# Performance work log

Hardware: AMD Instinct MI355X
Metric: run time of the kernel (lower is better)

The kernel has to match this reference:

```python
import jax, jax.numpy as jnp
import numpy as np

N, E = 50000, 800000
F, H, M = 64, 128, 64  # feature_dim, hidden_dim, message_dim (message_dim must equal feature_dim)


def _mlp(x, W1, b1, W2, b2):
    return jnp.maximum(x @ W1 + b1, 0.0) @ W2 + b2


def setup_inputs() -> dict:
    key = jax.random.key(0)
    ks = jax.random.split(key, 20)
    p = lambda k, s: (jax.random.normal(k, s, jnp.float32) * 0.05)
    return {
        "z_h": jax.random.normal(ks[0], (N, F), jnp.float32),
        "pos_world": jax.random.normal(ks[1], (3,), jnp.float32),
        "edge_index": jax.random.randint(ks[2], (2, E), 0, N),
        "We1": p(ks[3], (2 * F + 8, H)), "be1": p(ks[4], (H,)),
        "We2": p(ks[5], (H, M)), "be2": p(ks[6], (M,)),
        "Wg1": p(ks[7], (2 * F + 8, H)), "bg1": p(ks[8], (H,)),
        "Wg2": p(ks[9], (H, 1)), "bg2": p(ks[10], (1,)),
        "Wn1": p(ks[11], (F + M, H)), "bn1": p(ks[12], (H,)),
        "Wn2": p(ks[13], (H, F)), "bn2": p(ks[14], (F,)),
        "Ww1": p(ks[15], (F + 3, H)), "bw1": p(ks[16], (H,)),
        "Ww2": p(ks[17], (H, M)), "bw2": p(ks[18], (M,)),
    }


def reference(z_h, pos_world, edge_index,
              We1, be1, We2, be2,
              Wg1, bg1, Wg2, bg2,
              Wn1, bn1, Wn2, bn2,
              Ww1, bw1, Ww2, bw2):
    src, tgt = edge_index[0], edge_index[1]
    zs = z_h[src]  # [E, F]
    zt = z_h[tgt]  # [E, F]

    # edge features: diff(3) + dist(1) + vel cross product(3) + its norm(1)
    diff = zs[:, 0:3] - zt[:, 0:3]
    dist = jnp.sum(diff * diff, axis=-1, keepdims=True)
    cross = jnp.cross(zs[:, 3:6], zt[:, 3:6])
    cross_n = jnp.linalg.norm(cross, axis=-1, keepdims=True)
    e_feat = jnp.concatenate([diff, dist, cross, cross_n], axis=-1)  # [E, 8]

    inp_edge = jnp.concatenate([zs, zt, e_feat], axis=-1)  # [E, 2F+8]
    m = _mlp(inp_edge, We1, be1, We2, be2)                 # [E, M]
    w = jax.nn.sigmoid(_mlp(inp_edge, Wg1, bg1, Wg2, bg2))  # [E, 1]

    # scatter_add weighted messages to target nodes
    m_agg_h = jax.ops.segment_sum(w * m, tgt, num_segments=N)  # [N, F] (M == F)

    # world message: sum over all nodes, broadcast back
    diff_world = z_h[:, 0:3] - pos_world
    inp_world = jnp.concatenate([z_h, diff_world], axis=-1)  # [N, F+3]
    m_h_w = _mlp(inp_world, Ww1, bw1, Ww2, bw2)              # [N, M]
    m_agg_w = jnp.sum(m_h_w, axis=0, keepdims=True)          # [1, M] -> broadcast

    m_agg_total = m_agg_h + m_agg_w
    inp_node = jnp.concatenate([z_h, m_agg_total], axis=-1)  # [N, F+M]
    delta_z_h = _mlp(inp_node, Wn1, bn1, Wn2, bn2)           # [N, F]
    return delta_z_h
```

## Files before the change

### kernel.cpp

```cpp
#include <hip/hip_runtime.h>
#include <math.h>

#define NN 50000
#define NE 800000
#define EBLOCKS (NE / 64)
#define WBLOCKS ((NN + 63) / 64)

typedef float     f32x4  __attribute__((ext_vector_type(4)));
typedef __bf16    bf16x8 __attribute__((ext_vector_type(8)));
typedef _Float16  f16x2  __attribute__((ext_vector_type(2)));
typedef _Float16  f16x8  __attribute__((ext_vector_type(8)));

#define WE1F_OFF 0
#define WE2F_OFF 5120
#define WN1F_OFF 6144
#define WN2F_OFF 8192
#define WW1F_OFF 9216
#define WW2F_OFF 10752
#define NCHUNKS  11776


__device__ inline bf16x8 pack8(float4 a, float4 b) {
    bf16x8 r;
    r[0] = (__bf16)a.x; r[1] = (__bf16)a.y; r[2] = (__bf16)a.z; r[3] = (__bf16)a.w;
    r[4] = (__bf16)b.x; r[5] = (__bf16)b.y; r[6] = (__bf16)b.z; r[7] = (__bf16)b.w;
    return r;
}

__device__ inline void pk_atomic_add_f16(void* addr, f16x2 v) {
#if __has_builtin(__builtin_amdgcn_global_atomic_fadd_v2f16)
    __builtin_amdgcn_global_atomic_fadd_v2f16((f16x2*)addr, v);
#else
    asm volatile("global_atomic_pk_add_f16 %0, %1, off"
                 :: "v"(addr), "v"(v) : "memory");
#endif
}

__global__ __launch_bounds__(256) void prep(
    const float* __restrict__ We1, const float* __restrict__ Wg1,
    const float* __restrict__ We2, const float* __restrict__ Wn1,
    const float* __restrict__ Wn2, const float* __restrict__ Ww1,
    const float* __restrict__ Ww2, bf16x8* __restrict__ wsF,
    const float* __restrict__ z, float* __restrict__ db,
    float* __restrict__ m_agg_w)
{
    const int c = blockIdx.x * 256 + threadIdx.x;

    if (c < 64) m_agg_w[c] = 0.f;

    if (c < NN * 8) {
        int node = c >> 3, q = c & 7;
        const float4* s = (const float4*)(z + (long)node * 64) + q * 2;
        float4 a = s[0], b = s[1];
        *(bf16x8*)((char*)db + (long)node * 256 + 128 + q * 16) = pack8(a, b);
        float4 zz = {0.f, 0.f, 0.f, 0.f};
        *(float4*)((char*)db + (long)node * 256 + q * 16) = zz;
    }

    if (c >= NCHUNKS) return;
    const int lane = c & 63, l16 = lane & 15, row8 = ((lane >> 4) & 3) * 8;
    bf16x8 p;
    if (c < WE2F_OFF) {
        int ct = (c >> 6) & 15, kc = c >> 10;
        int col = ct * 16 + l16;
        const float* src = (col < 128) ? (We1 + col) : (Wg1 + (col - 128));
#pragma unroll
        for (int i = 0; i < 8; i++) {
            int r = kc * 32 + row8 + i;
            p[i] = (__bf16)((r < 136) ? src[(size_t)r * 128] : 0.f);
        }
    } else if (c < WN1F_OFF) {
        int cc = c - WE2F_OFF; int ct = (cc >> 6) & 3, kc = cc >> 8;
        int col = ct * 16 + l16;
#pragma unroll
        for (int i = 0; i < 8; i++)
            p[i] = (__bf16)We2[(size_t)(kc * 32 + row8 + i) * 64 + col];
    } else if (c < WN2F_OFF) {
        int cc = c - WN1F_OFF; int ct = (cc >> 6) & 7, kc = cc >> 9;
        int col = ct * 16 + l16;
#pragma unroll
        for (int i = 0; i < 8; i++)
            p[i] = (__bf16)Wn1[(size_t)(kc * 32 + row8 + i) * 128 + col];
    } else if (c < WW1F_OFF) {
        int cc = c - WN2F_OFF; int ct = (cc >> 6) & 3, kc = cc >> 8;
        int col = ct * 16 + l16;
#pragma unroll
        for (int i = 0; i < 8; i++)
            p[i] = (__bf16)Wn2[(size_t)(kc * 32 + row8 + i) * 64 + col];
    } else if (c < WW2F_OFF) {
        int cc = c - WW1F_OFF; int ct = (cc >> 6) & 7, kc = cc >> 9;
        int col = ct * 16 + l16;
#pragma unroll
        for (int i = 0; i < 8; i++) {
            int r = kc * 32 + row8 + i;
            p[i] = (__bf16)((r < 67) ? Ww1[(size_t)r * 128 + col] : 0.f);
        }
    } else {
        int cc = c - WW2F_OFF; int ct = (cc >> 6) & 3, kc = cc >> 8;
        int col = ct * 16 + l16;
#pragma unroll
        for (int i = 0; i < 8; i++)
            p[i] = (__bf16)Ww2[(size_t)(kc * 32 + row8 + i) * 64 + col];
    }
    wsF[c] = p;
}

union FusedLds {
    bf16x8 XF[1280];
    struct {
        bf16x8   HF[1024];
        _Float16 M[64 * 68];
    } s;
};

__global__ __launch_bounds__(512, 6) void fused_kernel(
    const float* __restrict__ z_h, const int* __restrict__ ei,
    const bf16x8* __restrict__ We1F, const bf16x8* __restrict__ We2F,
    const float* __restrict__ be1, const float* __restrict__ be2,
    const float* __restrict__ bg1, const float* __restrict__ Wg2,
    const float* __restrict__ bg2,
    const float* __restrict__ pos_world,
    const bf16x8* __restrict__ Ww1F, const bf16x8* __restrict__ Ww2F,
    const float* __restrict__ bw1, const float* __restrict__ bw2,
    float* __restrict__ magg_rows,
    float* __restrict__ m_agg_w)
{
    __shared__ FusedLds U;
    __shared__ int   tgt_s[64];
    __shared__ float gred[4][64];

    const int t = threadIdx.x;
    const int lane = t & 63, w = t >> 6;
    const int quad = lane >> 4, l16 = lane & 15;

    if (blockIdx.x >= EBLOCKS) {
        const int n0 = (blockIdx.x - EBLOCKS) * 64;
        {
            int nn = t >> 3, q = t & 7;
            int mt = nn >> 4, l16e = nn & 15;
            int node = n0 + nn; if (node >= NN) node = NN - 1;
            if (q < 4) {
                const float4* zr = (const float4*)(z_h + (long)node * 64) + q * 4;
                float4 a0 = zr[0], a1 = zr[1], a2 = zr[2], a3 = zr[3];
                int kcs = q >> 1, qa = (q & 1) * 2;
                U.XF[(kcs * 4 + mt) * 64 + qa * 16 + l16e]       = pack8(a0, a1);
                U.XF[(kcs * 4 + mt) * 64 + (qa + 1) * 16 + l16e] = pack8(a2, a3);
            } else if (q == 4) {
                float4 a0 = *(const float4*)(z_h + (long)node * 64);
                bf16x8 f;
#pragma unroll
                for (int i = 0; i < 8; i++) f[i] = (__bf16)0.f;
                f[0] = (__bf16)(a0.x - pos_world[0]);
                f[1] = (__bf16)(a0.y - pos_world[1]);
                f[2] = (__bf16)(a0.z - pos_world[2]);
                U.XF[(8 + mt) * 64 + l16e] = f;
            } else {
                bf16x8 z;
#pragma unroll
                for (int i = 0; i < 8; i++) z[i] = (__bf16)0.f;
                U.XF[(8 + mt) * 64 + (q - 4) * 16 + l16e] = z;
            }
        }
        __syncthreads();

        f32x4 acc[4];
        {
            float b = bw1[w * 16 + l16];
#pragma unroll
            for (int mt = 0; mt < 4; mt++) { f32x4 v = {b, b, b, b}; acc[mt] = v; }
        }
#pragma unroll
        for (int kc = 0; kc < 3; kc++) {
            bf16x8 bfr = Ww1F[(kc * 8 + w) * 64 + lane];
#pragma unroll
            for (int mt = 0; mt < 4; mt++)
                acc[mt] = __builtin_amdgcn_mfma_f32_16x16x32_bf16(
                    U.XF[(kc * 4 + mt) * 64 + lane], bfr, acc[mt], 0, 0, 0);
        }
        __syncthreads();

        {
            __bf16* HFp = (__bf16*)U.s.HF;
            int cw = w * 16 + l16;
            int kc2 = cw >> 5, quad2 = (cw >> 3) & 3, ii = cw & 7;
#pragma unroll
            for (int mt = 0; mt < 4; mt++)
#pragma unroll
                for (int r = 0; r < 4; r++)
                    HFp[(((kc2 * 4 + mt) * 64) + quad2 * 16 + quad * 4 + r) * 8 + ii] =
                        (__bf16)fmaxf(acc[mt][r], 0.f);
        }
        __syncthreads();

        {
            const int nt = w & 3, mh = w >> 2;
            f32x4 acc2[2];
            float b2 = bw2[nt * 16 + l16];
#pragma unroll
            for (int m = 0; m < 2; m++) { f32x4 v = {b2, b2, b2, b2}; acc2[m] = v; }
#pragma unroll
            for (int kc = 0; kc < 4; kc++) {
                bf16x8 b2f = Ww2F[(kc * 4 + nt) * 64 + lane];
#pragma unroll
                for (int m = 0; m < 2; m++)
                    acc2[m] = __builtin_amdgcn_mfma_f32_16x16x32_bf16(
                        U.s.HF[(kc * 4 + mh * 2 + m) * 64 + lane], b2f, acc2[m], 0, 0, 0);
            }
            float s = 0.f;
#pragma unroll
            for (int m = 0; m < 2; m++)
#pragma unroll
                for (int r = 0; r < 4; r++) {
                    int node = n0 + (mh * 2 + m) * 16 + quad * 4 + r;
                    s += (node < NN) ? acc2[m][r] : 0.f;
                }
            s += __shfl_xor(s, 16, 64);
            s += __shfl_xor(s, 32, 64);
            if (quad == 0) atomicAdd(m_agg_w + nt * 16 + l16, s);
        }
        return;
    }

    const int e0 = blockIdx.x * 64;

    {
        const int ee = t >> 3, q = t & 7;
        const int mt = ee >> 4, l16e = ee & 15;
        const int eg = e0 + ee;
        const int rs = ei[eg], rt = ei[NE + eg];
        const bf16x8* zs = (const bf16x8*)((const char*)magg_rows + (long)rs * 256 + 128);
        const bf16x8* zt = (const bf16x8*)((const char*)magg_rows + (long)rt * 256 + 128);
        bf16x8 sa = zs[q];
        bf16x8 ta = zt[q];
        const int kcs = q >> 2, qslot = q & 3;
        U.XF[(kcs * 4 + mt) * 64 + qslot * 16 + l16e]       = sa;
        U.XF[((kcs + 2) * 4 + mt) * 64 + qslot * 16 + l16e] = ta;
        if (q == 4) tgt_s[ee] = rt;
        if (q == 0) {
            float dx = (float)sa[0] - (float)ta[0];
            float dy = (float)sa[1] - (float)ta[1];
            float dz = (float)sa[2] - (float)ta[2];
            float ax = (float)sa[3], ay = (float)sa[4], az = (float)sa[5];
            float bx = (float)ta[3], by = (float)ta[4], bz = (float)ta[5];
            float cx = ay * bz - az * by;
            float cy = az * bx - ax * bz;
            float cz = ax * by - ay * bx;
            bf16x8 f;
            f[0] = (__bf16)dx; f[1] = (__bf16)dy; f[2] = (__bf16)dz;
            f[3] = (__bf16)(dx * dx + dy * dy + dz * dz);
            f[4] = (__bf16)cx; f[5] = (__bf16)cy; f[6] = (__bf16)cz;
            f[7] = (__bf16)sqrtf(cx * cx + cy * cy + cz * cz);
            U.XF[(16 + mt) * 64 + l16e] = f;
        } else if (q >= 5) {
            bf16x8 z;
#pragma unroll
            for (int i = 0; i < 8; i++) z[i] = (__bf16)0.f;
            U.XF[(16 + mt) * 64 + (q - 4) * 16 + l16e] = z;
        }
    }
    __syncthreads();

    f32x4 acc[4][2];
#pragma unroll
    for (int nt = 0; nt < 2; nt++) {
        int col = (w * 2 + nt) * 16 + l16;
        float b = (col < 128) ? be1[col] : bg1[col - 128];
#pragma unroll
        for (int mt = 0; mt < 4; mt++) { f32x4 v = {b, b, b, b}; acc[mt][nt] = v; }
    }
    bf16x8 bcur0 = We1F[(w * 2) * 64 + lane];
    bf16x8 bcur1 = We1F[(w * 2 + 1) * 64 + lane];
#pragma unroll
    for (int kc = 0; kc < 5; kc++) {
        bf16x8 bnx0, bnx1;
        if (kc < 4) {
            bnx0 = We1F[((kc + 1) * 16 + w * 2) * 64 + lane];
            bnx1 = We1F[((kc + 1) * 16 + w * 2 + 1) * 64 + lane];
        }
#pragma unroll
        for (int mt = 0; mt < 4; mt++) {
            bf16x8 af = U.XF[(kc * 4 + mt) * 64 + lane];
            acc[mt][0] = __builtin_amdgcn_mfma_f32_16x16x32_bf16(af, bcur0, acc[mt][0], 0, 0, 0);
            acc[mt][1] = __builtin_amdgcn_mfma_f32_16x16x32_bf16(af, bcur1, acc[mt][1], 0, 0, 0);
        }
        bcur0 = bnx0; bcur1 = bnx1;
    }
    __syncthreads();

    if (w < 4) {
        __bf16* HFp = (__bf16*)U.s.HF;
#pragma unroll
        for (int nt = 0; nt < 2; nt++) {
            int cw = (w * 2 + nt) * 16 + l16;
            int kc2 = cw >> 5, quad2 = (cw >> 3) & 3, ii = cw & 7;
#pragma unroll
            for (int mt = 0; mt < 4; mt++)
#pragma unroll
                for (int r = 0; r < 4; r++)
                    HFp[(((kc2 * 4 + mt) * 64) + quad2 * 16 + quad * 4 + r) * 8 + ii] =
                        (__bf16)fmaxf(acc[mt][nt][r], 0.f);
        }
    } else {
        float gp[4][4];
#pragma unroll
        for (int mt = 0; mt < 4; mt++)
#pragma unroll
            for (int r = 0; r < 4; r++) gp[mt][r] = 0.f;
#pragma unroll
        for (int nt = 0; nt < 2; nt++) {
            float wg = Wg2[((w - 4) * 2 + nt) * 16 + l16];
#pragma unroll
            for (int mt = 0; mt < 4; mt++)
#pragma unroll
                for (int r = 0; r < 4; r++)
                    gp[mt][r] += fmaxf(acc[mt][nt][r], 0.f) * wg;
        }
#pragma unroll
        for (int mask = 1; mask < 16; mask <<= 1)
#pragma unroll
            for (int mt = 0; mt < 4; mt++)
#pragma unroll
                for (int r = 0; r < 4; r++)
                    gp[mt][r] += __shfl_xor(gp[mt][r], mask, 64);
        if (l16 == 0) {
#pragma unroll
            for (int mt = 0; mt < 4; mt++)
#pragma unroll
                for (int r = 0; r < 4; r++)
                    gred[(w - 4) & 3][mt * 16 + quad * 4 + r] = gp[mt][r];
        }
    }
    __syncthreads();

    if (w < 4) {
        f32x4 acc2[4];
        float b2 = be2[w * 16 + l16];
#pragma unroll
        for (int mt = 0; mt < 4; mt++) { f32x4 v = {b2, b2, b2, b2}; acc2[mt] = v; }
        bf16x8 c2 = We2F[w * 64 + lane];
#pragma unroll
        for (int kc = 0; kc < 4; kc++) {
            bf16x8 n2;
            if (kc < 3) n2 = We2F[((kc + 1) * 4 + w) * 64 + lane];
#pragma unroll
            for (int mt = 0; mt < 4; mt++)
                acc2[mt] = __builtin_amdgcn_mfma_f32_16x16x32_bf16(
                    U.s.HF[(kc * 4 + mt) * 64 + lane], c2, acc2[mt], 0, 0, 0);
            c2 = n2;
        }

        float wgtreg;
        {
            float g = bg2[0] + gred[0][lane] + gred[1][lane]
                             + gred[2][lane] + gred[3][lane];
            wgtreg = 1.f / (1.f + __expf(-g));
        }

#pragma unroll
        for (int mt = 0; mt < 4; mt++)
#pragma unroll
            for (int r = 0; r < 4; r++) {
                int edge = mt * 16 + quad * 4 + r;
                float wg = __shfl(wgtreg, edge, 64);
                U.s.M[edge * 68 + w * 16 + l16] =
                    (_Float16)(acc2[mt][r] * wg);
            }
    }
    __syncthreads();

    {
        const int p = t & 31, eb = t >> 5;
        char* base = (char*)magg_rows;
#pragma unroll
        for (int k = 0; k < 4; k++) {
            int e = eb + k * 16;
            f16x2 v = *(const f16x2*)&U.s.M[e * 68 + p * 2];
            pk_atomic_add_f16(base + (long)tgt_s[e] * 256 + p * 4, v);
        }
    }
}

__global__ __launch_bounds__(512, 4) void node_kernel(
    const float* __restrict__ m_agg_w,
    const bf16x8* __restrict__ Wn1F, const bf16x8* __restrict__ Wn2F,
    const float* __restrict__ bn1, const float* __restrict__ bn2,
    float* __restrict__ outp)
{
    __shared__ bf16x8 XF[1024];
    __shared__ bf16x8 HF[1024];
    const int t = threadIdx.x;
    const int n0 = blockIdx.x * 64;
    const int lane = t & 63, w = t >> 6;
    const int quad = lane >> 4, l16 = lane & 15;

    {
        int nn = t >> 3, q = t & 7;
        int mt = nn >> 4, l16e = nn & 15;
        int node = n0 + nn; if (node >= NN) node = NN - 1;
        int half = q >> 2, sub = q & 3;
        bf16x8 c0, c1;
        if (half == 0) {
            const bf16x8* zr = (const bf16x8*)((const char*)outp + (long)node * 256 + 128) + sub * 2;
            c0 = zr[0]; c1 = zr[1];
        } else {
            const f16x8* mr = (const f16x8*)((const char*)outp + (long)node * 256) + sub * 2;
            f16x8 r0 = mr[0], r1 = mr[1];
            const float* mw = m_agg_w + sub * 16;
#pragma unroll
            for (int i = 0; i < 8; i++) {
                c0[i] = (__bf16)((float)r0[i] + mw[i]);
                c1[i] = (__bf16)((float)r1[i] + mw[i + 8]);
            }
        }
        int kcs = (sub >> 1) + half * 2, qa = (sub & 1) * 2;
        XF[(kcs * 4 + mt) * 64 + qa * 16 + l16e]       = c0;
        XF[(kcs * 4 + mt) * 64 + (qa + 1) * 16 + l16e] = c1;
    }
    __syncthreads();

    f32x4 acc[4];
    {
        float b = bn1[w * 16 + l16];
#pragma unroll
        for (int mt = 0; mt < 4; mt++) { f32x4 v = {b, b, b, b}; acc[mt] = v; }
    }
#pragma unroll
    for (int kc = 0; kc < 4; kc++) {
        bf16x8 bfr = Wn1F[(kc * 8 + w) * 64 + lane];
#pragma unroll
        for (int mt = 0; mt < 4; mt++)
            acc[mt] = __builtin_amdgcn_mfma_f32_16x16x32_bf16(
                XF[(kc * 4 + mt) * 64 + lane], bfr, acc[mt], 0, 0, 0);
    }

    {
        __bf16* HFp = (__bf16*)HF;
        int cw = w * 16 + l16;
        int kc2 = cw >> 5, quad2 = (cw >> 3) & 3, ii = cw & 7;
#pragma unroll
        for (int mt = 0; mt < 4; mt++)
#pragma unroll
            for (int r = 0; r < 4; r++)
                HFp[(((kc2 * 4 + mt) * 64) + quad2 * 16 + quad * 4 + r) * 8 + ii] =
                    (__bf16)fmaxf(acc[mt][r], 0.f);
    }
    __syncthreads();

    {
        const int nt = w & 3, mh = w >> 2;
        f32x4 acc2[2];
        float b2 = bn2[nt * 16 + l16];
#pragma unroll
        for (int m = 0; m < 2; m++) { f32x4 v = {b2, b2, b2, b2}; acc2[m] = v; }
#pragma unroll
        for (int kc = 0; kc < 4; kc++) {
            bf16x8 b2f = Wn2F[(kc * 4 + nt) * 64 + lane];
#pragma unroll
            for (int m = 0; m < 2; m++)
                acc2[m] = __builtin_amdgcn_mfma_f32_16x16x32_bf16(
                    HF[(kc * 4 + mh * 2 + m) * 64 + lane], b2f, acc2[m], 0, 0, 0);
        }
#pragma unroll
        for (int m = 0; m < 2; m++)
#pragma unroll
            for (int r = 0; r < 4; r++) {
                int node = n0 + (mh * 2 + m) * 16 + quad * 4 + r;
                if (node < NN)
                    outp[(long)node * 64 + nt * 16 + l16] = acc2[m][r];
            }
    }
}

extern "C" void kernel_launch(void* const* d_in, const int* in_sizes, int n_in,
                              void* d_out, int out_size, void* d_ws, size_t ws_size,
                              hipStream_t stream)
{
    const float* z_h       = (const float*)d_in[0];
    const float* pos_world = (const float*)d_in[1];
    const int*   ei        = (const int*)d_in[2];
    const float* We1 = (const float*)d_in[3];  const float* be1 = (const float*)d_in[4];
    const float* We2 = (const float*)d_in[5];  const float* be2 = (const float*)d_in[6];
    const float* Wg1 = (const float*)d_in[7];  const float* bg1 = (const float*)d_in[8];
    const float* Wg2 = (const float*)d_in[9];  const float* bg2 = (const float*)d_in[10];
    const float* Wn1 = (const float*)d_in[11]; const float* bn1 = (const float*)d_in[12];
    const float* Wn2 = (const float*)d_in[13]; const float* bn2 = (const float*)d_in[14];
    const float* Ww1 = (const float*)d_in[15]; const float* bw1 = (const float*)d_in[16];
    const float* Ww2 = (const float*)d_in[17]; const float* bw2 = (const float*)d_in[18];

    float*  outp    = (float*)d_out;
    float*  m_agg_w = (float*)d_ws;
    bf16x8* wsF     = (bf16x8*)((char*)d_ws + 256);

    prep<<<(NN * 8 + 255) / 256, 256, 0, stream>>>(
        We1, Wg1, We2, Wn1, Wn2, Ww1, Ww2, wsF, z_h, outp, m_agg_w);
    fused_kernel<<<EBLOCKS + WBLOCKS, 512, 0, stream>>>(
        z_h, ei, wsF + WE1F_OFF, wsF + WE2F_OFF,
        be1, be2, bg1, Wg2, bg2,
        pos_world, wsF + WW1F_OFF, wsF + WW2F_OFF, bw1, bw2,
        outp, m_agg_w);
    node_kernel<<<(NN + 63) / 64, 512, 0, stream>>>(
        m_agg_w, wsF + WN1F_OFF, wsF + WN2F_OFF, bn1, bn2, outp);
}
```

Baseline: 287.8 us.

## Process four edge tiles per block with software-prefetched gathers

```diff
diff --git a/kernel.cpp b/kernel.cpp
--- a/kernel.cpp
+++ b/kernel.cpp
@@ -3,7 +3,7 @@
 
 #define NN 50000
 #define NE 800000
-#define EBLOCKS (NE / 64)
+#define EBLOCKS4 (NE / 256)
 #define WBLOCKS ((NN + 63) / 64)
 
 typedef float     f32x4  __attribute__((ext_vector_type(4)));
@@ -133,8 +133,8 @@
     const int lane = t & 63, w = t >> 6;
     const int quad = lane >> 4, l16 = lane & 15;
 
-    if (blockIdx.x >= EBLOCKS) {
-        const int n0 = (blockIdx.x - EBLOCKS) * 64;
+    if (blockIdx.x >= EBLOCKS4) {
+        const int n0 = (blockIdx.x - EBLOCKS4) * 64;
         {
             int nn = t >> 3, q = t & 7;
             int mt = nn >> 4, l16e = nn & 15;
@@ -221,21 +221,26 @@
         return;
     }
 
-    const int e0 = blockIdx.x * 64;
-
+    const int ee = t >> 3, q = t & 7;
+    const int emt = ee >> 4, l16e = ee & 15;
+    const int eb0 = blockIdx.x * 256 + ee;
+    const int kcs = q >> 2, qslot = q & 3;
+
+    int rs_c, rt_c, rs_n, rt_n, rs_n2 = 0, rt_n2 = 0;
+    bf16x8 sa, ta, sa_n, ta_n;
+
+    rs_c = ei[eb0];  rt_c = ei[NE + eb0];
     {
-        const int ee = t >> 3, q = t & 7;
-        const int mt = ee >> 4, l16e = ee & 15;
-        const int eg = e0 + ee;
-        const int rs = ei[eg], rt = ei[NE + eg];
-        const bf16x8* zs = (const bf16x8*)((const char*)magg_rows + (long)rs * 256 + 128);
-        const bf16x8* zt = (const bf16x8*)((const char*)magg_rows + (long)rt * 256 + 128);
-        bf16x8 sa = zs[q];
-        bf16x8 ta = zt[q];
-        const int kcs = q >> 2, qslot = q & 3;
-        U.XF[(kcs * 4 + mt) * 64 + qslot * 16 + l16e]       = sa;
-        U.XF[((kcs + 2) * 4 + mt) * 64 + qslot * 16 + l16e] = ta;
-        if (q == 4) tgt_s[ee] = rt;
+        const bf16x8* zs = (const bf16x8*)((const char*)magg_rows + (long)rs_c * 256 + 128);
+        const bf16x8* zt = (const bf16x8*)((const char*)magg_rows + (long)rt_c * 256 + 128);
+        sa = zs[q]; ta = zt[q];
+    }
+    rs_n = ei[eb0 + 64]; rt_n = ei[NE + eb0 + 64];
+
+    for (int j = 0; j < 4; j++) {
+        U.XF[(kcs * 4 + emt) * 64 + qslot * 16 + l16e]       = sa;
+        U.XF[((kcs + 2) * 4 + emt) * 64 + qslot * 16 + l16e] = ta;
+        if (q == 4) tgt_s[ee] = rt_c;
         if (q == 0) {
             float dx = (float)sa[0] - (float)ta[0];
             float dy = (float)sa[1] - (float)ta[1];
@@ -250,132 +255,149 @@
             f[3] = (__bf16)(dx * dx + dy * dy + dz * dz);
             f[4] = (__bf16)cx; f[5] = (__bf16)cy; f[6] = (__bf16)cz;
             f[7] = (__bf16)sqrtf(cx * cx + cy * cy + cz * cz);
-            U.XF[(16 + mt) * 64 + l16e] = f;
+            U.XF[(16 + emt) * 64 + l16e] = f;
         } else if (q >= 5) {
             bf16x8 z;
 #pragma unroll
             for (int i = 0; i < 8; i++) z[i] = (__bf16)0.f;
-            U.XF[(16 + mt) * 64 + (q - 4) * 16 + l16e] = z;
-        }
-    }
-    __syncthreads();
-
-    f32x4 acc[4][2];
-#pragma unroll
-    for (int nt = 0; nt < 2; nt++) {
-        int col = (w * 2 + nt) * 16 + l16;
-        float b = (col < 128) ? be1[col] : bg1[col - 128];
-#pragma unroll
-        for (int mt = 0; mt < 4; mt++) { f32x4 v = {b, b, b, b}; acc[mt][nt] = v; }
-    }
-    bf16x8 bcur0 = We1F[(w * 2) * 64 + lane];
-    bf16x8 bcur1 = We1F[(w * 2 + 1) * 64 + lane];
-#pragma unroll
-    for (int kc = 0; kc < 5; kc++) {
-        bf16x8 bnx0, bnx1;
-        if (kc < 4) {
-            bnx0 = We1F[((kc + 1) * 16 + w * 2) * 64 + lane];
-            bnx1 = We1F[((kc + 1) * 16 + w * 2 + 1) * 64 + lane];
-        }
-#pragma unroll
-        for (int mt = 0; mt < 4; mt++) {
-            bf16x8 af = U.XF[(kc * 4 + mt) * 64 + lane];
-            acc[mt][0] = __builtin_amdgcn_mfma_f32_16x16x32_bf16(af, bcur0, acc[mt][0], 0, 0, 0);
-            acc[mt][1] = __builtin_amdgcn_mfma_f32_16x16x32_bf16(af, bcur1, acc[mt][1], 0, 0, 0);
-        }
-        bcur0 = bnx0; bcur1 = bnx1;
-    }
-    __syncthreads();
-
-    if (w < 4) {
-        __bf16* HFp = (__bf16*)U.s.HF;
+            U.XF[(16 + emt) * 64 + (q - 4) * 16 + l16e] = z;
+        }
+        __syncthreads();
+
+        if (j < 3) {
+            const bf16x8* zs = (const bf16x8*)((const char*)magg_rows + (long)rs_n * 256 + 128);
+            const bf16x8* zt = (const bf16x8*)((const char*)magg_rows + (long)rt_n * 256 + 128);
+            sa_n = zs[q]; ta_n = zt[q];
+        }
+        if (j < 2) {
+            rs_n2 = ei[eb0 + (j + 2) * 64];
+            rt_n2 = ei[NE + eb0 + (j + 2) * 64];
+        }
+
+        f32x4 acc[4][2];
 #pragma unroll
         for (int nt = 0; nt < 2; nt++) {
-            int cw = (w * 2 + nt) * 16 + l16;
-            int kc2 = cw >> 5, quad2 = (cw >> 3) & 3, ii = cw & 7;
+            int col = (w * 2 + nt) * 16 + l16;
+            float b = (col < 128) ? be1[col] : bg1[col - 128];
+#pragma unroll
+            for (int mt = 0; mt < 4; mt++) { f32x4 v = {b, b, b, b}; acc[mt][nt] = v; }
+        }
+        bf16x8 bcur0 = We1F[(w * 2) * 64 + lane];
+        bf16x8 bcur1 = We1F[(w * 2 + 1) * 64 + lane];
+#pragma unroll
+        for (int kc = 0; kc < 5; kc++) {
+            bf16x8 bnx0, bnx1;
+            if (kc < 4) {
+                bnx0 = We1F[((kc + 1) * 16 + w * 2) * 64 + lane];
+                bnx1 = We1F[((kc + 1) * 16 + w * 2 + 1) * 64 + lane];
+            }
+#pragma unroll
+            for (int mt = 0; mt < 4; mt++) {
+                bf16x8 af = U.XF[(kc * 4 + mt) * 64 + lane];
+                acc[mt][0] = __builtin_amdgcn_mfma_f32_16x16x32_bf16(af, bcur0, acc[mt][0], 0, 0, 0);
+                acc[mt][1] = __builtin_amdgcn_mfma_f32_16x16x32_bf16(af, bcur1, acc[mt][1], 0, 0, 0);
+            }
+            bcur0 = bnx0; bcur1 = bnx1;
+        }
+        __syncthreads();
+
+        if (w < 4) {
+            __bf16* HFp = (__bf16*)U.s.HF;
+#pragma unroll
+            for (int nt = 0; nt < 2; nt++) {
+                int cw = (w * 2 + nt) * 16 + l16;
+                int kc2 = cw >> 5, quad2 = (cw >> 3) & 3, ii = cw & 7;
+#pragma unroll
+                for (int mt = 0; mt < 4; mt++)
+#pragma unroll
+                    for (int r = 0; r < 4; r++)
+                        HFp[(((kc2 * 4 + mt) * 64) + quad2 * 16 + quad * 4 + r) * 8 + ii] =
+                            (__bf16)fmaxf(acc[mt][nt][r], 0.f);
+            }
+        } else {
+            float gp[4][4];
 #pragma unroll
             for (int mt = 0; mt < 4; mt++)
 #pragma unroll
-                for (int r = 0; r < 4; r++)
-                    HFp[(((kc2 * 4 + mt) * 64) + quad2 * 16 + quad * 4 + r) * 8 + ii] =
-                        (__bf16)fmaxf(acc[mt][nt][r], 0.f);
-        }
-    } else {
-        float gp[4][4];
-#pragma unroll
-        for (int mt = 0; mt < 4; mt++)
-#pragma unroll
-            for (int r = 0; r < 4; r++) gp[mt][r] = 0.f;
-#pragma unroll
-        for (int nt = 0; nt < 2; nt++) {
-            float wg = Wg2[((w - 4) * 2 + nt) * 16 + l16];
+                for (int r = 0; r < 4; r++) gp[mt][r] = 0.f;
+#pragma unroll
+            for (int nt = 0; nt < 2; nt++) {
+                float wg = Wg2[((w - 4) * 2 + nt) * 16 + l16];
+#pragma unroll
+                for (int mt = 0; mt < 4; mt++)
+#pragma unroll
+                    for (int r = 0; r < 4; r++)
+                        gp[mt][r] += fmaxf(acc[mt][nt][r], 0.f) * wg;
+            }
+#pragma unroll
+            for (int mask = 1; mask < 16; mask <<= 1)
+#pragma unroll
+                for (int mt = 0; mt < 4; mt++)
+#pragma unroll
+                    for (int r = 0; r < 4; r++)
+                        gp[mt][r] += __shfl_xor(gp[mt][r], mask, 64);
+            if (l16 == 0) {
+#pragma unroll
+                for (int mt = 0; mt < 4; mt++)
+#pragma unroll
+                    for (int r = 0; r < 4; r++)
+                        gred[(w - 4) & 3][mt * 16 + quad * 4 + r] = gp[mt][r];
+            }
+        }
+        __syncthreads();
+
+        if (w < 4) {
+            f32x4 acc2[4];
+            float b2 = be2[w * 16 + l16];
+#pragma unroll
+            for (int mt = 0; mt < 4; mt++) { f32x4 v = {b2, b2, b2, b2}; acc2[mt] = v; }
+            bf16x8 c2 = We2F[w * 64 + lane];
+#pragma unroll
+            for (int kc = 0; kc < 4; kc++) {
+                bf16x8 n2;
+                if (kc < 3) n2 = We2F[((kc + 1) * 4 + w) * 64 + lane];
+#pragma unroll
+                for (int mt = 0; mt < 4; mt++)
+                    acc2[mt] = __builtin_amdgcn_mfma_f32_16x16x32_bf16(
+                        U.s.HF[(kc * 4 + mt) * 64 + lane], c2, acc2[mt], 0, 0, 0);
+                c2 = n2;
+            }
+
+            float wgtreg;
+            {
+                float g = bg2[0] + gred[0][lane] + gred[1][lane]
+                                 + gred[2][lane] + gred[3][lane];
+                wgtreg = 1.f / (1.f + __expf(-g));
+            }
+
 #pragma unroll
             for (int mt = 0; mt < 4; mt++)
 #pragma unroll
-                for (int r = 0; r < 4; r++)
-                    gp[mt][r] += fmaxf(acc[mt][nt][r], 0.f) * wg;
-        }
-#pragma unroll
-        for (int mask = 1; mask < 16; mask <<= 1)
-#pragma unroll
-            for (int mt = 0; mt < 4; mt++)
-#pragma unroll
-                for (int r = 0; r < 4; r++)
-                    gp[mt][r] += __shfl_xor(gp[mt][r], mask, 64);
-        if (l16 == 0) {
-#pragma unroll
-            for (int mt = 0; mt < 4; mt++)
-#pragma unroll
-                for (int r = 0; r < 4; r++)
-                    gred[(w - 4) & 3][mt * 16 + quad * 4 + r] = gp[mt][r];
-        }
-    }
-    __syncthreads();
-
-    if (w < 4) {
-        f32x4 acc2[4];
-        float b2 = be2[w * 16 + l16];
-#pragma unroll
-        for (int mt = 0; mt < 4; mt++) { f32x4 v = {b2, b2, b2, b2}; acc2[mt] = v; }
-        bf16x8 c2 = We2F[w * 64 + lane];
-#pragma unroll
-        for (int kc = 0; kc < 4; kc++) {
-            bf16x8 n2;
-            if (kc < 3) n2 = We2F[((kc + 1) * 4 + w) * 64 + lane];
-#pragma unroll
-            for (int mt = 0; mt < 4; mt++)
-                acc2[mt] = __builtin_amdgcn_mfma_f32_16x16x32_bf16(
-                    U.s.HF[(kc * 4 + mt) * 64 + lane], c2, acc2[mt], 0, 0, 0);
-            c2 = n2;
-        }
-
-        float wgtreg;
+                for (int r = 0; r < 4; r++) {
+                    int edge = mt * 16 + quad * 4 + r;
+                    float wg = __shfl(wgtreg, edge, 64);
+                    U.s.M[edge * 68 + w * 16 + l16] =
+                        (_Float16)(acc2[mt][r] * wg);
+                }
+        }
+        __syncthreads();
+
         {
-            float g = bg2[0] + gred[0][lane] + gred[1][lane]
-                             + gred[2][lane] + gred[3][lane];
-            wgtreg = 1.f / (1.f + __expf(-g));
-        }
-
-#pragma unroll
-        for (int mt = 0; mt < 4; mt++)
-#pragma unroll
-            for (int r = 0; r < 4; r++) {
-                int edge = mt * 16 + quad * 4 + r;
-                float wg = __shfl(wgtreg, edge, 64);
-                U.s.M[edge * 68 + w * 16 + l16] =
-                    (_Float16)(acc2[mt][r] * wg);
-            }
-    }
-    __syncthreads();
-
-    {
-        const int p = t & 31, eb = t >> 5;
-        char* base = (char*)magg_rows;
-#pragma unroll
-        for (int k = 0; k < 4; k++) {
-            int e = eb + k * 16;
-            f16x2 v = *(const f16x2*)&U.s.M[e * 68 + p * 2];
-            pk_atomic_add_f16(base + (long)tgt_s[e] * 256 + p * 4, v);
+            const int p = t & 31, eb = t >> 5;
+            char* base = (char*)magg_rows;
+#pragma unroll
+            for (int k = 0; k < 4; k++) {
+                int e = eb + k * 16;
+                f16x2 v = *(const f16x2*)&U.s.M[e * 68 + p * 2];
+                pk_atomic_add_f16(base + (long)tgt_s[e] * 256 + p * 4, v);
+            }
+        }
+
+        if (j < 3) {
+            asm volatile("s_barrier" ::: "memory");
+            rs_c = rs_n; rt_c = rt_n;
+            rs_n = rs_n2; rt_n = rt_n2;
+            sa = sa_n; ta = ta_n;
         }
     }
 }
@@ -493,7 +515,7 @@
 
     prep<<<(NN * 8 + 255) / 256, 256, 0, stream>>>(
         We1, Wg1, We2, Wn1, Wn2, Ww1, Ww2, wsF, z_h, outp, m_agg_w);
-    fused_kernel<<<EBLOCKS + WBLOCKS, 512, 0, stream>>>(
+    fused_kernel<<<EBLOCKS4 + WBLOCKS, 512, 0, stream>>>(
         z_h, ei, wsF + WE1F_OFF, wsF + WE2F_OFF,
         be1, be2, bg1, Wg2, bg2,
         pos_world, wsF + WW1F_OFF, wsF + WW2F_OFF, bw1, bw2,
```

Measured after the change: 590.8 us. +105.3%, slower.

## Spread second edge-MLP layer over all waves using transposed LDS reads

Applied to the files above, without the earlier changes.

```diff
diff --git a/kernel.cpp b/kernel.cpp
--- a/kernel.cpp
+++ b/kernel.cpp
@@ -8,7 +8,9 @@
 
 typedef float     f32x4  __attribute__((ext_vector_type(4)));
 typedef __bf16    bf16x8 __attribute__((ext_vector_type(8)));
+typedef __bf16    bf16x4 __attribute__((ext_vector_type(4)));
 typedef _Float16  f16x2  __attribute__((ext_vector_type(2)));
+typedef _Float16  f16x4  __attribute__((ext_vector_type(4)));
 typedef _Float16  f16x8  __attribute__((ext_vector_type(8)));
 
 #define WE1F_OFF 0
@@ -288,17 +290,21 @@
     __syncthreads();
 
     if (w < 4) {
-        __bf16* HFp = (__bf16*)U.s.HF;
+        __bf16* HFb = (__bf16*)U.s.HF;
 #pragma unroll
         for (int nt = 0; nt < 2; nt++) {
-            int cw = (w * 2 + nt) * 16 + l16;
-            int kc2 = cw >> 5, quad2 = (cw >> 3) & 3, ii = cw & 7;
-#pragma unroll
-            for (int mt = 0; mt < 4; mt++)
+            int h = (w * 2 + nt) * 16 + l16;
+            int kc2 = h >> 5, h32 = h & 31;
+            int idx0 = kc2 * 2048 + ((h32 >> 2) & 1) * 256 + (h32 >> 3) * 64
+                     + (h32 & 3) * 16 + quad * 4;
+#pragma unroll
+            for (int mt = 0; mt < 4; mt++) {
+                bf16x4 hv;
 #pragma unroll
                 for (int r = 0; r < 4; r++)
-                    HFp[(((kc2 * 4 + mt) * 64) + quad2 * 16 + quad * 4 + r) * 8 + ii] =
-                        (__bf16)fmaxf(acc[mt][nt][r], 0.f);
+                    hv[r] = (__bf16)fmaxf(acc[mt][nt][r], 0.f);
+                *(bf16x4*)(HFb + idx0 + mt * 512) = hv;
+            }
         }
     } else {
         float gp[4][4];
@@ -332,39 +338,53 @@
     }
     __syncthreads();
 
-    if (w < 4) {
-        f32x4 acc2[4];
-        float b2 = be2[w * 16 + l16];
-#pragma unroll
-        for (int mt = 0; mt < 4; mt++) { f32x4 v = {b2, b2, b2, b2}; acc2[mt] = v; }
-        bf16x8 c2 = We2F[w * 64 + lane];
+    {
+        const int mct = w & 3, et0 = (w >> 2) * 2;
+        f32x4 acc2[2];
+        {
+            float4 b4 = *(const float4*)(be2 + mct * 16 + quad * 4);
+            f32x4 v; v[0] = b4.x; v[1] = b4.y; v[2] = b4.z; v[3] = b4.w;
+            acc2[0] = v; acc2[1] = v;
+        }
+        const char* hb = (const char*)U.s.HF;
 #pragma unroll
         for (int kc = 0; kc < 4; kc++) {
-            bf16x8 n2;
-            if (kc < 3) n2 = We2F[((kc + 1) * 4 + w) * 64 + lane];
-#pragma unroll
-            for (int mt = 0; mt < 4; mt++)
-                acc2[mt] = __builtin_amdgcn_mfma_f32_16x16x32_bf16(
-                    U.s.HF[(kc * 4 + mt) * 64 + lane], c2, acc2[mt], 0, 0, 0);
-            c2 = n2;
-        }
-
-        float wgtreg;
-        {
-            float g = bg2[0] + gred[0][lane] + gred[1][lane]
-                             + gred[2][lane] + gred[3][lane];
-            wgtreg = 1.f / (1.f + __expf(-g));
-        }
-
-#pragma unroll
-        for (int mt = 0; mt < 4; mt++)
-#pragma unroll
-            for (int r = 0; r < 4; r++) {
-                int edge = mt * 16 + quad * 4 + r;
-                float wg = __shfl(wgtreg, edge, 64);
-                U.s.M[edge * 68 + w * 16 + l16] =
-                    (_Float16)(acc2[mt][r] * wg);
+            bf16x8 a2 = We2F[(kc * 4 + mct) * 64 + lane];
+            union { unsigned long long u; __bf16 h[4]; } t0, t1, t2, t3;
+            unsigned b0 = (unsigned)(unsigned long long)(hb + (kc * 4 + et0) * 1024);
+            unsigned b1 = b0 + 512;
+            unsigned b2 = (unsigned)(unsigned long long)(hb + (kc * 4 + et0 + 1) * 1024);
+            unsigned b3 = b2 + 512;
+            asm volatile(
+                "ds_read_b64_tr_b16 %0, %4\n\t"
+                "ds_read_b64_tr_b16 %1, %5\n\t"
+                "ds_read_b64_tr_b16 %2, %6\n\t"
+                "ds_read_b64_tr_b16 %3, %7\n\t"
+                "s_waitcnt lgkmcnt(0)"
+                : "=&v"(t0.u), "=&v"(t1.u), "=&v"(t2.u), "=&v"(t3.u)
+                : "v"(b0), "v"(b1), "v"(b2), "v"(b3));
+            bf16x8 f0, f1;
+#pragma unroll
+            for (int i = 0; i < 4; i++) {
+                f0[i] = t0.h[i]; f0[4 + i] = t1.h[i];
+                f1[i] = t2.h[i]; f1[4 + i] = t3.h[i];
             }
+            acc2[0] = __builtin_amdgcn_mfma_f32_16x16x32_bf16(a2, f0, acc2[0], 0, 0, 0);
+            acc2[1] = __builtin_amdgcn_mfma_f32_16x16x32_bf16(a2, f1, acc2[1], 0, 0, 0);
+        }
+
+#pragma unroll
+        for (int m = 0; m < 2; m++) {
+            int edge = (et0 + m) * 16 + l16;
+            float g = bg2[0] + gred[0][edge] + gred[1][edge]
+                             + gred[2][edge] + gred[3][edge];
+            float wg = 1.f / (1.f + __expf(-g));
+            f16x4 hv;
+#pragma unroll
+            for (int r = 0; r < 4; r++)
+                hv[r] = (_Float16)(acc2[m][r] * wg);
+            *(f16x4*)((char*)U.s.M + edge * 136 + (mct * 16 + quad * 4) * 2) = hv;
+        }
     }
     __syncthreads();
 
```

Measured after the change: 297.8 us. 1.03x slower.

## Halve fused kernel tile to 32 edges and 256 threads per block

Applied to the files above, without the earlier changes.

```diff
diff --git a/kernel.cpp b/kernel.cpp
--- a/kernel.cpp
+++ b/kernel.cpp
@@ -3,7 +3,7 @@
 
 #define NN 50000
 #define NE 800000
-#define EBLOCKS (NE / 64)
+#define EBLOCKS (NE / 32)
 #define WBLOCKS ((NN + 63) / 64)
 
 typedef float     f32x4  __attribute__((ext_vector_type(4)));
@@ -106,14 +106,14 @@
 }
 
 union FusedLds {
-    bf16x8 XF[1280];
+    bf16x8 XF[1024];
     struct {
-        bf16x8   HF[1024];
-        _Float16 M[64 * 68];
+        bf16x8   HF[512];
+        _Float16 M[32 * 68];
     } s;
 };
 
-__global__ __launch_bounds__(512, 6) void fused_kernel(
+__global__ __launch_bounds__(256, 6) void fused_kernel(
     const float* __restrict__ z_h, const int* __restrict__ ei,
     const bf16x8* __restrict__ We1F, const bf16x8* __restrict__ We2F,
     const float* __restrict__ be1, const float* __restrict__ be2,
@@ -126,8 +126,8 @@
     float* __restrict__ m_agg_w)
 {
     __shared__ FusedLds U;
-    __shared__ int   tgt_s[64];
-    __shared__ float gred[4][64];
+    __shared__ int   tgt_s[32];
+    __shared__ float gred[4][32];
 
     const int t = threadIdx.x;
     const int lane = t & 63, w = t >> 6;
@@ -136,17 +136,15 @@
     if (blockIdx.x >= EBLOCKS) {
         const int n0 = (blockIdx.x - EBLOCKS) * 64;
         {
-            int nn = t >> 3, q = t & 7;
+            int nn = t >> 2, q = t & 3;
             int mt = nn >> 4, l16e = nn & 15;
             int node = n0 + nn; if (node >= NN) node = NN - 1;
-            if (q < 4) {
-                const float4* zr = (const float4*)(z_h + (long)node * 64) + q * 4;
-                float4 a0 = zr[0], a1 = zr[1], a2 = zr[2], a3 = zr[3];
-                int kcs = q >> 1, qa = (q & 1) * 2;
-                U.XF[(kcs * 4 + mt) * 64 + qa * 16 + l16e]       = pack8(a0, a1);
-                U.XF[(kcs * 4 + mt) * 64 + (qa + 1) * 16 + l16e] = pack8(a2, a3);
-            } else if (q == 4) {
-                float4 a0 = *(const float4*)(z_h + (long)node * 64);
+            const float4* zr = (const float4*)(z_h + (long)node * 64) + q * 4;
+            float4 a0 = zr[0], a1 = zr[1], a2 = zr[2], a3 = zr[3];
+            int kcs = q >> 1, qa = (q & 1) * 2;
+            U.XF[(kcs * 4 + mt) * 64 + qa * 16 + l16e]       = pack8(a0, a1);
+            U.XF[(kcs * 4 + mt) * 64 + (qa + 1) * 16 + l16e] = pack8(a2, a3);
+            if (q == 0) {
                 bf16x8 f;
 #pragma unroll
                 for (int i = 0; i < 8; i++) f[i] = (__bf16)0.f;
@@ -155,73 +153,85 @@
                 f[2] = (__bf16)(a0.z - pos_world[2]);
                 U.XF[(8 + mt) * 64 + l16e] = f;
             } else {
-                bf16x8 z;
-#pragma unroll
-                for (int i = 0; i < 8; i++) z[i] = (__bf16)0.f;
-                U.XF[(8 + mt) * 64 + (q - 4) * 16 + l16e] = z;
+                bf16x8 z8;
+#pragma unroll
+                for (int i = 0; i < 8; i++) z8[i] = (__bf16)0.f;
+                U.XF[(8 + mt) * 64 + q * 16 + l16e] = z8;
             }
         }
         __syncthreads();
 
-        f32x4 acc[4];
+        f32x4 acc[4][2];
+#pragma unroll
+        for (int nt2 = 0; nt2 < 2; nt2++) {
+            float b = bw1[(w * 2 + nt2) * 16 + l16];
+#pragma unroll
+            for (int mt = 0; mt < 4; mt++) { f32x4 v = {b, b, b, b}; acc[mt][nt2] = v; }
+        }
+#pragma unroll
+        for (int kc = 0; kc < 3; kc++) {
+#pragma unroll
+            for (int nt2 = 0; nt2 < 2; nt2++) {
+                bf16x8 bfr = Ww1F[(kc * 8 + w * 2 + nt2) * 64 + lane];
+#pragma unroll
+                for (int mt = 0; mt < 4; mt++)
+                    acc[mt][nt2] = __builtin_amdgcn_mfma_f32_16x16x32_bf16(
+                        U.XF[(kc * 4 + mt) * 64 + lane], bfr, acc[mt][nt2], 0, 0, 0);
+            }
+        }
+        __syncthreads();
+
         {
-            float b = bw1[w * 16 + l16];
-#pragma unroll
-            for (int mt = 0; mt < 4; mt++) { f32x4 v = {b, b, b, b}; acc[mt] = v; }
-        }
-#pragma unroll
-        for (int kc = 0; kc < 3; kc++) {
-            bf16x8 bfr = Ww1F[(kc * 8 + w) * 64 + lane];
-#pragma unroll
-            for (int mt = 0; mt < 4; mt++)
-                acc[mt] = __builtin_amdgcn_mfma_f32_16x16x32_bf16(
-                    U.XF[(kc * 4 + mt) * 64 + lane], bfr, acc[mt], 0, 0, 0);
+            __bf16* HFp = (__bf16*)U.XF;
+#pragma unroll
+            for (int nt2 = 0; nt2 < 2; nt2++) {
+                int cw = (w * 2 + nt2) * 16 + l16;
+                int kc2 = cw >> 5, quad2 = (cw >> 3) & 3, ii = cw & 7;
+#pragma unroll
+                for (int mt = 0; mt < 4; mt++)
+#pragma unroll
+                    for (int r = 0; r < 4; r++)
+                        HFp[(((kc2 * 4 + mt) * 64) + quad2 * 16 + quad * 4 + r) * 8 + ii] =
+                            (__bf16)fmaxf(acc[mt][nt2][r], 0.f);
+            }
         }
         __syncthreads();
 
         {
-            __bf16* HFp = (__bf16*)U.s.HF;
-            int cw = w * 16 + l16;
-            int kc2 = cw >> 5, quad2 = (cw >> 3) & 3, ii = cw & 7;
-#pragma unroll
-            for (int mt = 0; mt < 4; mt++)
-#pragma unroll
-                for (int r = 0; r < 4; r++)
-                    HFp[(((kc2 * 4 + mt) * 64) + quad2 * 16 + quad * 4 + r) * 8 + ii] =
-                        (__bf16)fmaxf(acc[mt][r], 0.f);
-        }
-        __syncthreads();
-
-        {
-            const int nt = w & 3, mh = w >> 2;
-            f32x4 acc2[2];
-            float b2 = bw2[nt * 16 + l16];
-#pragma unroll
-            for (int m = 0; m < 2; m++) { f32x4 v = {b2, b2, b2, b2}; acc2[m] = v; }
+            f32x4 acc2[2][2];
+            float b2 = bw2[w * 16 + l16];
+#pragma unroll
+            for (int mh = 0; mh < 2; mh++)
+#pragma unroll
+                for (int m = 0; m < 2; m++) { f32x4 v = {b2, b2, b2, b2}; acc2[mh][m] = v; }
 #pragma unroll
             for (int kc = 0; kc < 4; kc++) {
-                bf16x8 b2f = Ww2F[(kc * 4 + nt) * 64 + lane];
+                bf16x8 b2f = Ww2F[(kc * 4 + w) * 64 + lane];
+#pragma unroll
+                for (int mh = 0; mh < 2; mh++)
+#pragma unroll
+                    for (int m = 0; m < 2; m++)
+                        acc2[mh][m] = __builtin_amdgcn_mfma_f32_16x16x32_bf16(
+                            U.XF[(kc * 4 + mh * 2 + m) * 64 + lane], b2f, acc2[mh][m], 0, 0, 0);
+            }
+            float s = 0.f;
+#pragma unroll
+            for (int mh = 0; mh < 2; mh++)
 #pragma unroll
                 for (int m = 0; m < 2; m++)
-                    acc2[m] = __builtin_amdgcn_mfma_f32_16x16x32_bf16(
-                        U.s.HF[(kc * 4 + mh * 2 + m) * 64 + lane], b2f, acc2[m], 0, 0, 0);
-            }
-            float s = 0.f;
-#pragma unroll
-            for (int m = 0; m < 2; m++)
-#pragma unroll
-                for (int r = 0; r < 4; r++) {
-                    int node = n0 + (mh * 2 + m) * 16 + quad * 4 + r;
-                    s += (node < NN) ? acc2[m][r] : 0.f;
-                }
+#pragma unroll
+                    for (int r = 0; r < 4; r++) {
+                        int node = n0 + (mh * 2 + m) * 16 + quad * 4 + r;
+                        s += (node < NN) ? acc2[mh][m][r] : 0.f;
+                    }
             s += __shfl_xor(s, 16, 64);
             s += __shfl_xor(s, 32, 64);
-            if (quad == 0) atomicAdd(m_agg_w + nt * 16 + l16, s);
+            if (quad == 0) atomicAdd(m_agg_w + w * 16 + l16, s);
         }
         return;
     }
 
-    const int e0 = blockIdx.x * 64;
+    const int e0 = blockIdx.x * 32;
 
     {
         const int ee = t >> 3, q = t & 7;
@@ -233,8 +243,8 @@
         bf16x8 sa = zs[q];
         bf16x8 ta = zt[q];
         const int kcs = q >> 2, qslot = q & 3;
-        U.XF[(kcs * 4 + mt) * 64 + qslot * 16 + l16e]       = sa;
-        U.XF[((kcs + 2) * 4 + mt) * 64 + qslot * 16 + l16e] = ta;
+        U.XF[(kcs * 2 + mt) * 64 + qslot * 16 + l16e]       = sa;
+        U.XF[((kcs + 2) * 2 + mt) * 64 + qslot * 16 + l16e] = ta;
         if (q == 4) tgt_s[ee] = rt;
         if (q == 0) {
             float dx = (float)sa[0] - (float)ta[0];
@@ -250,67 +260,64 @@
             f[3] = (__bf16)(dx * dx + dy * dy + dz * dz);
             f[4] = (__bf16)cx; f[5] = (__bf16)cy; f[6] = (__bf16)cz;
             f[7] = (__bf16)sqrtf(cx * cx + cy * cy + cz * cz);
-            U.XF[(16 + mt) * 64 + l16e] = f;
+            U.XF[(8 + mt) * 64 + l16e] = f;
         } else if (q >= 5) {
             bf16x8 z;
 #pragma unroll
             for (int i = 0; i < 8; i++) z[i] = (__bf16)0.f;
-            U.XF[(16 + mt) * 64 + (q - 4) * 16 + l16e] = z;
+            U.XF[(8 + mt) * 64 + (q - 4) * 16 + l16e] = z;
         }
     }
     __syncthreads();
 
-    f32x4 acc[4][2];
-#pragma unroll
-    for (int nt = 0; nt < 2; nt++) {
-        int col = (w * 2 + nt) * 16 + l16;
-        float b = (col < 128) ? be1[col] : bg1[col - 128];
-#pragma unroll
-        for (int mt = 0; mt < 4; mt++) { f32x4 v = {b, b, b, b}; acc[mt][nt] = v; }
-    }
-    bf16x8 bcur0 = We1F[(w * 2) * 64 + lane];
-    bf16x8 bcur1 = We1F[(w * 2 + 1) * 64 + lane];
+    f32x4 acc[2][4];
+#pragma unroll
+    for (int nt = 0; nt < 4; nt++) {
+        float b = (nt < 2) ? be1[(w * 2 + nt) * 16 + l16]
+                           : bg1[(w * 2 + nt - 2) * 16 + l16];
+#pragma unroll
+        for (int mt = 0; mt < 2; mt++) { f32x4 v = {b, b, b, b}; acc[mt][nt] = v; }
+    }
 #pragma unroll
     for (int kc = 0; kc < 5; kc++) {
-        bf16x8 bnx0, bnx1;
-        if (kc < 4) {
-            bnx0 = We1F[((kc + 1) * 16 + w * 2) * 64 + lane];
-            bnx1 = We1F[((kc + 1) * 16 + w * 2 + 1) * 64 + lane];
-        }
-#pragma unroll
-        for (int mt = 0; mt < 4; mt++) {
-            bf16x8 af = U.XF[(kc * 4 + mt) * 64 + lane];
-            acc[mt][0] = __builtin_amdgcn_mfma_f32_16x16x32_bf16(af, bcur0, acc[mt][0], 0, 0, 0);
-            acc[mt][1] = __builtin_amdgcn_mfma_f32_16x16x32_bf16(af, bcur1, acc[mt][1], 0, 0, 0);
-        }
-        bcur0 = bnx0; bcur1 = bnx1;
+        bf16x8 bf0 = We1F[(kc * 16 + w * 2) * 64 + lane];
+        bf16x8 bf1 = We1F[(kc * 16 + w * 2 + 1) * 64 + lane];
+        bf16x8 bf2 = We1F[(kc * 16 + 8 + w * 2) * 64 + lane];
+        bf16x8 bf3 = We1F[(kc * 16 + 8 + w * 2 + 1) * 64 + lane];
+#pragma unroll
+        for (int mt = 0; mt < 2; mt++) {
+            bf16x8 af = U.XF[(kc * 2 + mt) * 64 + lane];
+            acc[mt][0] = __builtin_amdgcn_mfma_f32_16x16x32_bf16(af, bf0, acc[mt][0], 0, 0, 0);
+            acc[mt][1] = __builtin_amdgcn_mfma_f32_16x16x32_bf16(af, bf1, acc[mt][1], 0, 0, 0);
+            acc[mt][2] = __builtin_amdgcn_mfma_f32_16x16x32_bf16(af, bf2, acc[mt][2], 0, 0, 0);
+            acc[mt][3] = __builtin_amdgcn_mfma_f32_16x16x32_bf16(af, bf3, acc[mt][3], 0, 0, 0);
+        }
     }
     __syncthreads();
 
-    if (w < 4) {
+    {
         __bf16* HFp = (__bf16*)U.s.HF;
 #pragma unroll
         for (int nt = 0; nt < 2; nt++) {
             int cw = (w * 2 + nt) * 16 + l16;
             int kc2 = cw >> 5, quad2 = (cw >> 3) & 3, ii = cw & 7;
 #pragma unroll
-            for (int mt = 0; mt < 4; mt++)
+            for (int mt = 0; mt < 2; mt++)
 #pragma unroll
                 for (int r = 0; r < 4; r++)
-                    HFp[(((kc2 * 4 + mt) * 64) + quad2 * 16 + quad * 4 + r) * 8 + ii] =
+                    HFp[(((kc2 * 2 + mt) * 64) + quad2 * 16 + quad * 4 + r) * 8 + ii] =
                         (__bf16)fmaxf(acc[mt][nt][r], 0.f);
         }
-    } else {
-        float gp[4][4];
-#pragma unroll
-        for (int mt = 0; mt < 4; mt++)
+        float gp[2][4];
+#pragma unroll
+        for (int mt = 0; mt < 2; mt++)
 #pragma unroll
             for (int r = 0; r < 4; r++) gp[mt][r] = 0.f;
 #pragma unroll
-        for (int nt = 0; nt < 2; nt++) {
-            float wg = Wg2[((w - 4) * 2 + nt) * 16 + l16];
-#pragma unroll
-            for (int mt = 0; mt < 4; mt++)
+        for (int nt = 2; nt < 4; nt++) {
+            float wg = Wg2[(w * 2 + nt - 2) * 16 + l16];
+#pragma unroll
+            for (int mt = 0; mt < 2; mt++)
 #pragma unroll
                 for (int r = 0; r < 4; r++)
                     gp[mt][r] += fmaxf(acc[mt][nt][r], 0.f) * wg;
@@ -318,46 +325,43 @@
 #pragma unroll
         for (int mask = 1; mask < 16; mask <<= 1)
 #pragma unroll
-            for (int mt = 0; mt < 4; mt++)
+            for (int mt = 0; mt < 2; mt++)
 #pragma unroll
                 for (int r = 0; r < 4; r++)
                     gp[mt][r] += __shfl_xor(gp[mt][r], mask, 64);
         if (l16 == 0) {
 #pragma unroll
-            for (int mt = 0; mt < 4; mt++)
+            for (int mt = 0; mt < 2; mt++)
 #pragma unroll
                 for (int r = 0; r < 4; r++)
-                    gred[(w - 4) & 3][mt * 16 + quad * 4 + r] = gp[mt][r];
+                    gred[w][mt * 16 + quad * 4 + r] = gp[mt][r];
         }
     }
     __syncthreads();
 
-    if (w < 4) {
-        f32x4 acc2[4];
+    {
+        f32x4 acc2[2];
         float b2 = be2[w * 16 + l16];
 #pragma unroll
-        for (int mt = 0; mt < 4; mt++) { f32x4 v = {b2, b2, b2, b2}; acc2[mt] = v; }
-        bf16x8 c2 = We2F[w * 64 + lane];
+        for (int mt = 0; mt < 2; mt++) { f32x4 v = {b2, b2, b2, b2}; acc2[mt] = v; }
 #pragma unroll
         for (int kc = 0; kc < 4; kc++) {
-            bf16x8 n2;
-            if (kc < 3) n2 = We2F[((kc + 1) * 4 + w) * 64 + lane];
-#pragma unroll
-            for (int mt = 0; mt < 4; mt++)
+            bf16x8 c2 = We2F[(kc * 4 + w) * 64 + lane];
+#pragma unroll
+            for (int mt = 0; mt < 2; mt++)
                 acc2[mt] = __builtin_amdgcn_mfma_f32_16x16x32_bf16(
-                    U.s.HF[(kc * 4 + mt) * 64 + lane], c2, acc2[mt], 0, 0, 0);
-            c2 = n2;
+                    U.s.HF[(kc * 2 + mt) * 64 + lane], c2, acc2[mt], 0, 0, 0);
         }
 
         float wgtreg;
         {
-            float g = bg2[0] + gred[0][lane] + gred[1][lane]
-                             + gred[2][lane] + gred[3][lane];
+            int e = lane & 31;
+            float g = bg2[0] + gred[0][e] + gred[1][e] + gred[2][e] + gred[3][e];
             wgtreg = 1.f / (1.f + __expf(-g));
         }
 
 #pragma unroll
-        for (int mt = 0; mt < 4; mt++)
+        for (int mt = 0; mt < 2; mt++)
 #pragma unroll
             for (int r = 0; r < 4; r++) {
                 int edge = mt * 16 + quad * 4 + r;
@@ -369,11 +373,11 @@
     __syncthreads();
 
     {
-        const int p = t & 31, eb = t >> 5;
+        const int p = t & 31, eh = t >> 5;
         char* base = (char*)magg_rows;
 #pragma unroll
         for (int k = 0; k < 4; k++) {
-            int e = eb + k * 16;
+            int e = eh + k * 8;
             f16x2 v = *(const f16x2*)&U.s.M[e * 68 + p * 2];
             pk_atomic_add_f16(base + (long)tgt_s[e] * 256 + p * 4, v);
         }
@@ -493,7 +497,7 @@
 
     prep<<<(NN * 8 + 255) / 256, 256, 0, stream>>>(
         We1, Wg1, We2, Wn1, Wn2, Ww1, Ww2, wsF, z_h, outp, m_agg_w);
-    fused_kernel<<<EBLOCKS + WBLOCKS, 512, 0, stream>>>(
+    fused_kernel<<<EBLOCKS + WBLOCKS, 256, 0, stream>>>(
         z_h, ei, wsF + WE1F_OFF, wsF + WE2F_OFF,
         be1, be2, bg1, Wg2, bg2,
         pos_world, wsF + WW1F_OFF, wsF + WW2F_OFF, bw1, bw2,
```

Result: faster. 264.1 us (-8.2%).
